# Kernel optimization log

Measured on AMD Instinct MI355X. Metric: run time of the kernel, lower is better.

Reference implementation:

```python
import jax, jax.numpy as jnp
import numpy as np

N_NODES = 8192
N_EDGES = 524288
N_PAIRS = 262144
N_TYPES = 86


def _gcn_conv(x, W, b, src, dst, n):
    # PyG GCNConv: transform, add self-loops, symmetric degree normalization,
    # scatter-add aggregation at destination nodes.
    xw = x @ W  # [N, F_out]
    loop = jnp.arange(n, dtype=src.dtype)
    s = jnp.concatenate([src, loop])
    d = jnp.concatenate([dst, loop])
    deg = jax.ops.segment_sum(jnp.ones(d.shape, xw.dtype), d, num_segments=n)
    dinv = jnp.where(deg > 0, jax.lax.rsqrt(deg), 0.0)  # deg^{-1/2}, 0 for isolated
    coef = dinv[s] * dinv[d]  # [E+N]
    out = jax.ops.segment_sum(xw[s] * coef[:, None], d, num_segments=n)
    return out + b


def setup_inputs() -> dict:
    key = jax.random.key(0)
    ks = jax.random.split(key, 10)
    x = jax.random.normal(ks[0], (N_NODES, N_NODES), dtype=jnp.float32)
    edge_index = jax.random.randint(ks[1], (2, N_EDGES), 0, N_NODES, dtype=jnp.int32)
    drug1_idx = jax.random.randint(ks[2], (N_PAIRS,), 0, N_NODES, dtype=jnp.int32)
    drug2_idx = jax.random.randint(ks[3], (N_PAIRS,), 0, N_NODES, dtype=jnp.int32)
    W1 = jax.random.normal(ks[4], (N_NODES, 128), dtype=jnp.float32) / np.sqrt(N_NODES)
    b1 = jnp.zeros((128,), jnp.float32)
    W2 = jax.random.normal(ks[5], (128, 64), dtype=jnp.float32) / np.sqrt(128.0)
    b2 = jnp.zeros((64,), jnp.float32)
    Wfc = jax.random.normal(ks[6], (128, N_TYPES), dtype=jnp.float32) / np.sqrt(128.0)
    bfc = jnp.zeros((N_TYPES,), jnp.float32)
    return {"x": x, "edge_index": edge_index, "drug1_idx": drug1_idx,
            "drug2_idx": drug2_idx, "W1": W1, "b1": b1, "W2": W2, "b2": b2,
            "Wfc": Wfc, "bfc": bfc}


def reference(x, edge_index, drug1_idx, drug2_idx, W1, b1, W2, b2, Wfc, bfc):
    n = x.shape[0]
    src, dst = edge_index[0], edge_index[1]
    h = jax.nn.relu(_gcn_conv(x, W1, b1, src, dst, n))
    # dropout p=0.3 is identity at inference (training=False)
    h = jax.nn.relu(_gcn_conv(h, W2, b2, src, dst, n))
    combined = jnp.concatenate([h[drug1_idx], h[drug2_idx]], axis=1)  # [P, 128]
    return jax.nn.sigmoid(combined @ Wfc + bfc)
```

## Files before the change

### kernel.cpp

```cpp
#include <hip/hip_runtime.h>
#include <math.h>
#include <stdint.h>
#include <stddef.h>

#define N_NODES 8192
#define N_EDGES 524288
#define N_PAIRS 262144
#define N_TYPES 86
#define F1 128
#define F2 64

typedef unsigned short ushort_t;
typedef unsigned int uint_t;
typedef __attribute__((ext_vector_type(8))) short bfrag;
typedef __attribute__((ext_vector_type(4))) float ffrag;

typedef __attribute__((address_space(3))) char lds_char;
typedef __attribute__((address_space(1))) const char g_char;

__device__ __forceinline__ void gload16(const void* g, void* l) {
  __builtin_amdgcn_global_load_lds((const g_char*)g, (lds_char*)l, 16, 0, 0);
}

__device__ inline ushort_t f2bf(float f) {
  uint_t u = __float_as_uint(f);
  uint_t r = u + 0x7fffu + ((u >> 16) & 1u);
  return (ushort_t)(r >> 16);
}
__device__ inline float bf2f(ushort_t h) {
  return __uint_as_float(((uint_t)h) << 16);
}


__global__ void zero_k(int* __restrict__ p) {
  p[blockIdx.x * 256 + threadIdx.x] = 0;
}

__global__ void count_deg_k(const int* __restrict__ dst, int* __restrict__ cnt) {
  int e = blockIdx.x * blockDim.x + threadIdx.x;
  if (e < N_EDGES) atomicAdd(&cnt[dst[e]], 1);
}

__global__ void scan_k(const int* __restrict__ cnt, int* __restrict__ rp,
                       int* __restrict__ fill, float* __restrict__ dinv) {
  __shared__ int s[1024];
  int t = threadIdx.x;
  int v[8];
  int sum = 0;
#pragma unroll
  for (int i = 0; i < 8; i++) {
    v[i] = cnt[t * 8 + i];
    dinv[t * 8 + i] = 1.0f / sqrtf((float)(v[i] + 1));
    sum += v[i];
  }
  s[t] = sum;
  __syncthreads();
  for (int off = 1; off < 1024; off <<= 1) {
    int add = (t >= off) ? s[t - off] : 0;
    __syncthreads();
    s[t] += add;
    __syncthreads();
  }
  int excl = s[t] - sum;
#pragma unroll
  for (int i = 0; i < 8; i++) {
    rp[t * 8 + i] = excl;
    fill[t * 8 + i] = excl;
    excl += v[i];
  }
  if (t == 1023) rp[N_NODES] = excl;
}

__global__ void scatter_k(const int* __restrict__ src, const int* __restrict__ dst,
                          int* fill, int* __restrict__ csr) {
  int e = blockIdx.x * blockDim.x + threadIdx.x;
  if (e < N_EDGES) {
    int d = dst[e];
    int pos = atomicAdd(&fill[d], 1);
    csr[pos] = src[e];
  }
}


__global__ __launch_bounds__(256) void w1split_k(const float* __restrict__ W1,
                                                 ushort_t* __restrict__ W1th,
                                                 ushort_t* __restrict__ W1tl) {
  __shared__ ushort_t lh[32 * 65];
  __shared__ ushort_t ll[32 * 65];
  int tid = threadIdx.x;
  int k0 = blockIdx.x * 64;
  int n0 = blockIdx.y * 32;
#pragma unroll
  for (int i = 0; i < 8; i++) {
    int c = tid + 256 * i;
    int kr = c >> 5, nc = c & 31;
    float v = W1[(size_t)(k0 + kr) * F1 + n0 + nc];
    ushort_t h = f2bf(v);
    ushort_t l = f2bf(v - bf2f(h));
    lh[nc * 65 + kr] = h;
    ll[nc * 65 + kr] = l;
  }
  __syncthreads();
#pragma unroll
  for (int i = 0; i < 2; i++) {
    int c = tid + 256 * i;
    int buf = c >> 8;
    int cc = c & 255;
    int nr = cc >> 3, kc = cc & 7;
    const ushort_t* l = buf ? ll : lh;
    uint4 u;
    u.x = (uint_t)l[nr * 65 + kc * 8 + 0] | ((uint_t)l[nr * 65 + kc * 8 + 1] << 16);
    u.y = (uint_t)l[nr * 65 + kc * 8 + 2] | ((uint_t)l[nr * 65 + kc * 8 + 3] << 16);
    u.z = (uint_t)l[nr * 65 + kc * 8 + 4] | ((uint_t)l[nr * 65 + kc * 8 + 5] << 16);
    u.w = (uint_t)l[nr * 65 + kc * 8 + 6] | ((uint_t)l[nr * 65 + kc * 8 + 7] << 16);
    ushort_t* dst = (buf ? W1tl : W1th) + (size_t)(n0 + nr) * N_NODES + k0 + kc * 8;
    *(uint4*)dst = u;
  }
}


#define OAH 0
#define OAL 4096
#define OBB(b) (8192 + (b) * 16384)

#define SCHED0 __builtin_amdgcn_sched_barrier(0)
#define WAITVM(N)  do { asm volatile("s_waitcnt vmcnt(" #N ")" ::: "memory"); SCHED0; } while (0)
#define WAITVML(N) do { asm volatile("s_waitcnt vmcnt(" #N ") lgkmcnt(0)" ::: "memory"); SCHED0; } while (0)

__global__ __launch_bounds__(256, 4) void gemm1_mfma_k(const float* __restrict__ x,
                                                       const ushort_t* __restrict__ W1th,
                                                       const ushort_t* __restrict__ W1tl,
                                                       float* __restrict__ part, int kspan) {
  __shared__ __align__(16) char lds[40960];
  int tid = threadIdx.x;
  int wave = tid >> 6, lane = tid & 63;
  int wr = wave >> 1, wc = wave & 1;
  int lrow = lane & 15, kgrp = lane >> 4;
  int m_blk = blockIdx.y * 64;
  int kbase = blockIdx.x * kspan;
  int ktiles = kspan >> 5;

  int bq = wave;
  int b_row = bq * 32 + (lane >> 2);
  int b_kel = ((lane & 3) ^ ((lane >> 2) & 3)) << 3;

  ffrag acc[2][4];
#pragma unroll
  for (int mi = 0; mi < 2; mi++)
#pragma unroll
    for (int ni = 0; ni < 4; ni++) acc[mi][ni] = (ffrag)(0.0f);

  float4 av[2];

#define LOADA(K0)                                                                    \
  {                                                                                  \
    _Pragma("unroll") for (int i = 0; i < 2; i++) {                                  \
      int c = tid + 256 * i;                                                         \
      int row = c >> 3, c4 = c & 7;                                                  \
      av[i] = *(const float4*)&x[(size_t)(m_blk + row) * N_NODES + (K0) + 4 * c4];   \
    }                                                                                \
  }

#define ISSUE_B(K0, BSEL)                                                            \
  {                                                                                  \
    _Pragma("unroll") for (int i = 0; i < 2; i++) {                                  \
      const ushort_t* gh = W1th + (size_t)(b_row + i * 16) * N_NODES + (K0) + b_kel; \
      gload16(gh, lds + OBB(BSEL) + bq * 2048 + i * 1024);                           \
      const ushort_t* gl = W1tl + (size_t)(b_row + i * 16) * N_NODES + (K0) + b_kel; \
      gload16(gl, lds + OBB(BSEL) + 8192 + bq * 2048 + i * 1024);                    \
    }                                                                                \
  }

#define STOREA()                                                                     \
  {                                                                                  \
    _Pragma("unroll") for (int i = 0; i < 2; i++) {                                  \
      int c = tid + 256 * i;                                                         \
      int row = c >> 3, c4 = c & 7;                                                  \
      float f0 = av[i].x, f1 = av[i].y, f2 = av[i].z, f3 = av[i].w;                  \
      ushort_t h0 = f2bf(f0), h1 = f2bf(f1), h2 = f2bf(f2), h3 = f2bf(f3);           \
      ushort_t l0 = f2bf(f0 - bf2f(h0)), l1 = f2bf(f1 - bf2f(h1));                   \
      ushort_t l2 = f2bf(f2 - bf2f(h2)), l3 = f2bf(f3 - bf2f(h3));                   \
      uint2 hp, lp;                                                                  \
      hp.x = (uint_t)h0 | ((uint_t)h1 << 16); hp.y = (uint_t)h2 | ((uint_t)h3 << 16);\
      lp.x = (uint_t)l0 | ((uint_t)l1 << 16); lp.y = (uint_t)l2 | ((uint_t)l3 << 16);\
      uint_t off = row * 64 + ((c4 * 8) ^ ((row & 3) << 4));                         \
      *(uint2*)(lds + OAH + off) = hp;                                               \
      *(uint2*)(lds + OAL + off) = lp;                                               \
    }                                                                                \
  }

#define COMPUTE(BSEL)                                                                \
  {                                                                                  \
    bfrag bh[4], bl[4];                                                              \
    _Pragma("unroll") for (int ni = 0; ni < 4; ni++) {                               \
      int brow = wc * 64 + ni * 16 + lrow;                                           \
      uint_t boff = brow * 64 + ((kgrp * 16) ^ ((brow & 3) << 4));                   \
      bh[ni] = *(const bfrag*)(lds + OBB(BSEL) + boff);                              \
      bl[ni] = *(const bfrag*)(lds + OBB(BSEL) + 8192 + boff);                       \
    }                                                                                \
    _Pragma("unroll") for (int mi = 0; mi < 2; mi++) {                               \
      int arow = wr * 32 + mi * 16 + lrow;                                           \
      uint_t aoff = arow * 64 + ((kgrp * 16) ^ ((arow & 3) << 4));                   \
      bfrag ah = *(const bfrag*)(lds + OAH + aoff);                                  \
      bfrag al = *(const bfrag*)(lds + OAL + aoff);                                  \
      _Pragma("unroll") for (int ni = 0; ni < 4; ni++) {                             \
        acc[mi][ni] = __builtin_amdgcn_mfma_f32_16x16x32_bf16(ah, bh[ni], acc[mi][ni], 0, 0, 0); \
        acc[mi][ni] = __builtin_amdgcn_mfma_f32_16x16x32_bf16(ah, bl[ni], acc[mi][ni], 0, 0, 0); \
        acc[mi][ni] = __builtin_amdgcn_mfma_f32_16x16x32_bf16(al, bh[ni], acc[mi][ni], 0, 0, 0); \
      }                                                                              \
    }                                                                                \
  }

  LOADA(kbase);
  ISSUE_B(kbase, 0);
  WAITVM(4);
  STOREA();
  WAITVML(0);
  __builtin_amdgcn_s_barrier();
  SCHED0;

  for (int s = 0; s < ktiles; ++s) {
    int more = (s + 1 < ktiles);
    if (more) {
      int k0n = kbase + ((s + 1) << 5);
      LOADA(k0n);
      SCHED0;
      ISSUE_B(k0n, (s + 1) & 1);
      SCHED0;
    }
    __builtin_amdgcn_s_setprio(1);
    COMPUTE(s & 1);
    __builtin_amdgcn_s_setprio(0);
    __builtin_amdgcn_s_barrier();
    SCHED0;
    if (more) {
      WAITVM(4);
      STOREA();
      WAITVML(0);
      __builtin_amdgcn_s_barrier();
      SCHED0;
    }
  }

  float* outp = part + (size_t)blockIdx.x * (N_NODES * F1);
#pragma unroll
  for (int mi = 0; mi < 2; mi++) {
#pragma unroll
    for (int ni = 0; ni < 4; ni++) {
      int col = wc * 64 + ni * 16 + lrow;
#pragma unroll
      for (int r = 0; r < 4; r++) {
        int row = m_blk + wr * 32 + mi * 16 + kgrp * 4 + r;
        outp[(size_t)row * F1 + col] = acc[mi][ni][r];
      }
    }
  }
#undef LOADA
#undef ISSUE_B
#undef STOREA
#undef COMPUTE
}

__global__ void reduceS_k(const float* __restrict__ part, float* __restrict__ xw1, int S) {
  int i = blockIdx.x * blockDim.x + threadIdx.x;
  float4 a = ((const float4*)part)[i];
  for (int s = 1; s < S; s++) {
    float4 b = ((const float4*)(part + (size_t)s * N_NODES * F1))[i];
    a.x += b.x; a.y += b.y; a.z += b.z; a.w += b.w;
  }
  ((float4*)xw1)[i] = a;
}


template <int F>
__global__ void agg_k(const float* __restrict__ xw, const int* __restrict__ csr,
                      const int* __restrict__ rp, const float* __restrict__ dinv,
                      const float* __restrict__ bias, float* __restrict__ hout) {
  int node = blockIdx.x;
  int f = threadIdx.x;
  __shared__ int sidx[F];
  __shared__ float sdv[F];
  int beg = rp[node], end = rp[node + 1];
  float acc = 0.f;
  for (int base = beg; base < end; base += F) {
    int n = end - base;
    if (n > F) n = F;
    __syncthreads();
    if (f < n) {
      int s = csr[base + f];
      sidx[f] = s;
      sdv[f] = dinv[s];
    }
    __syncthreads();
    for (int i = 0; i < n; i++) acc += xw[(size_t)sidx[i] * F + f] * sdv[i];
  }
  float dv = dinv[node];
  float v = (acc + xw[(size_t)node * F + f] * dv) * dv + bias[f];
  hout[(size_t)node * F + f] = v > 0.f ? v : 0.f;
}


__global__ __launch_bounds__(256) void gemm2_k(const float* __restrict__ h1,
                                               const float* __restrict__ W2,
                                               float* __restrict__ xw2) {
  __shared__ float W2s[F1 * F2];
  __shared__ float As[16 * F1];
  int tid = threadIdx.x;
  int r0 = blockIdx.x * 16;
#pragma unroll
  for (int j = 0; j < 8; j++)
    ((float4*)W2s)[tid + 256 * j] = ((const float4*)W2)[tid + 256 * j];
#pragma unroll
  for (int j = 0; j < 2; j++)
    ((float4*)As)[tid + 256 * j] = ((const float4*)(h1 + (size_t)r0 * F1))[tid + 256 * j];
  __syncthreads();
  int r = tid >> 4, c4 = tid & 15;
  float4 acc = make_float4(0.f, 0.f, 0.f, 0.f);
#pragma unroll 8
  for (int k = 0; k < F1; k++) {
    float a = As[r * F1 + k];
    float4 bv = *(float4*)&W2s[k * F2 + 4 * c4];
    acc.x += a * bv.x; acc.y += a * bv.y; acc.z += a * bv.z; acc.w += a * bv.w;
  }
  *(float4*)&xw2[(size_t)(r0 + r) * F2 + 4 * c4] = acc;
}


__global__ void pboth_k(const float* __restrict__ h2, const float* __restrict__ Wfc,
                        float* __restrict__ P) {
  __shared__ float hs[64 * 16];
  int tid = threadIdx.x;
  int r0 = blockIdx.x * 16;
  for (int idx = tid; idx < 256; idx += 192) {
    int row = idx >> 4, k4 = idx & 15;
    float4 h = *(const float4*)&h2[(size_t)(r0 + row) * F2 + 4 * k4];
    hs[(4 * k4 + 0) * 16 + row] = h.x;
    hs[(4 * k4 + 1) * 16 + row] = h.y;
    hs[(4 * k4 + 2) * 16 + row] = h.z;
    hs[(4 * k4 + 3) * 16 + row] = h.w;
  }
  __syncthreads();
  if (tid < 172) {
    int half = tid < 86 ? 0 : 1;
    int j = tid - 86 * half;
    const float* wp = Wfc + (size_t)(64 * half) * N_TYPES + j;
    float acc[16];
#pragma unroll
    for (int r = 0; r < 16; r++) acc[r] = 0.f;
    for (int k = 0; k < 64; k++) {
      float w = wp[(size_t)k * N_TYPES];
      const float* hk = &hs[k * 16];
#pragma unroll
      for (int r = 0; r < 16; r++) acc[r] += hk[r] * w;
    }
#pragma unroll
    for (int r = 0; r < 16; r++) P[(size_t)(r0 + r) * 172 + tid] = acc[r];
  }
}


__global__ void final_k(const float* __restrict__ P, const int* __restrict__ d1,
                        const int* __restrict__ d2, const float* __restrict__ bfc,
                        float* __restrict__ out) {
  int gid = blockIdx.x * blockDim.x + threadIdx.x;
  if (gid >= N_PAIRS * 43) return;
  int p = gid / 43;
  int j = gid - p * 43;
  int a = d1[p], b = d2[p];
  float2 v1 = *(const float2*)&P[(size_t)a * 172 + 2 * j];
  float2 v2 = *(const float2*)&P[(size_t)b * 172 + 86 + 2 * j];
  float2 bb = *(const float2*)&bfc[2 * j];
  float z0 = v1.x + v2.x + bb.x;
  float z1 = v1.y + v2.y + bb.y;
  float2 o;
  o.x = 1.0f / (1.0f + expf(-z0));
  o.y = 1.0f / (1.0f + expf(-z1));
  *(float2*)&out[(size_t)p * 86 + 2 * j] = o;
}


extern "C" void kernel_launch(void* const* d_in, const int* in_sizes, int n_in,
                              void* d_out, int out_size, void* d_ws, size_t ws_size,
                              hipStream_t stream) {
  const float* x   = (const float*)d_in[0];
  const int*   ei  = (const int*)d_in[1];
  const int*   d1  = (const int*)d_in[2];
  const int*   d2  = (const int*)d_in[3];
  const float* W1  = (const float*)d_in[4];
  const float* b1  = (const float*)d_in[5];
  const float* W2  = (const float*)d_in[6];
  const float* b2  = (const float*)d_in[7];
  const float* Wfc = (const float*)d_in[8];
  const float* bfc = (const float*)d_in[9];
  float* out = (float*)d_out;

  const int* esrc = ei;
  const int* edst = ei + N_EDGES;

  char* w = (char*)d_ws;
  size_t off = 0;
  auto alloc = [&](size_t bytes) -> char* {
    char* p = w + off;
    off += (bytes + 255) & ~(size_t)255;
    return p;
  };
  int*      cnt  = (int*)alloc((size_t)N_NODES * 4);
  float*    dinv = (float*)alloc((size_t)N_NODES * 4);
  int*      rp   = (int*)alloc((size_t)(N_NODES + 1) * 4);
  int*      fill = (int*)alloc((size_t)N_NODES * 4);
  int*      csr  = (int*)alloc((size_t)N_EDGES * 4);
  ushort_t* W1th = (ushort_t*)alloc((size_t)N_NODES * F1 * 2);
  ushort_t* W1tl = (ushort_t*)alloc((size_t)N_NODES * F1 * 2);
  float*    h1   = (float*)alloc((size_t)N_NODES * F1 * 4);
  float*    xw2  = (float*)alloc((size_t)N_NODES * F2 * 4);
  float*    h2   = (float*)alloc((size_t)N_NODES * F2 * 4);
  float*    P    = (float*)alloc((size_t)N_NODES * 172 * 4);

  size_t partBytes = (size_t)N_NODES * F1 * 4;
  int S = 8;
  while (S > 1 && off + (size_t)S * partBytes > ws_size) S >>= 1;
  float* part = (float*)alloc((size_t)S * partBytes);
  float* xw1 = part;
  if (off > ws_size) return;

  zero_k<<<N_NODES / 256, 256, 0, stream>>>(cnt);
  count_deg_k<<<N_EDGES / 256, 256, 0, stream>>>(edst, cnt);
  scan_k<<<1, 1024, 0, stream>>>(cnt, rp, fill, dinv);
  scatter_k<<<N_EDGES / 256, 256, 0, stream>>>(esrc, edst, fill, csr);

  w1split_k<<<dim3(N_NODES / 64, F1 / 32), 256, 0, stream>>>(W1, W1th, W1tl);
  gemm1_mfma_k<<<dim3(S, N_NODES / 64), 256, 0, stream>>>(x, W1th, W1tl, part, N_NODES / S);
  if (S > 1)
    reduceS_k<<<(N_NODES * F1 / 4) / 256, 256, 0, stream>>>(part, xw1, S);
  agg_k<F1><<<N_NODES, F1, 0, stream>>>(xw1, csr, rp, dinv, b1, h1);

  gemm2_k<<<N_NODES / 16, 256, 0, stream>>>(h1, W2, xw2);
  agg_k<F2><<<N_NODES, F2, 0, stream>>>(xw2, csr, rp, dinv, b2, h2);

  pboth_k<<<N_NODES / 16, 192, 0, stream>>>(h2, Wfc, P);
  final_k<<<(N_PAIRS * 43 + 255) / 256, 256, 0, stream>>>(P, d1, d2, bfc, out);
}
```

Before: 286.0 us.

## Restructure gemm1 into 128-wide K groups with 4-deep B pipeline

The first GEMM now uses 32-row M tiles and loads A in 128-wide K groups, splitting each to bf16 hi/lo once per group. B tiles go into four LDS slots that are prefetched asynchronously, which cuts barriers and lets global loads overlap several compute steps. Each block's starting K group is rotated by block index to spread memory traffic. The cost is twice the LDS (lower occupancy, launch bounds 2) and a grid twice as large, so the W1 B tiles are reloaded by more blocks.

```diff
diff --git a/kernel.cpp b/kernel.cpp
--- a/kernel.cpp
+++ b/kernel.cpp
@@ -119,91 +119,99 @@
 }
 
 
-#define OAH 0
-#define OAL 4096
-#define OBB(b) (8192 + (b) * 16384)
+#define ALDS_H 0
+#define ALDS_L 8192
+#define BLDS(j) (16384 + ((j) & 3) * 16384)
 
 #define SCHED0 __builtin_amdgcn_sched_barrier(0)
 #define WAITVM(N)  do { asm volatile("s_waitcnt vmcnt(" #N ")" ::: "memory"); SCHED0; } while (0)
-#define WAITVML(N) do { asm volatile("s_waitcnt vmcnt(" #N ") lgkmcnt(0)" ::: "memory"); SCHED0; } while (0)
-
-__global__ __launch_bounds__(256, 4) void gemm1_mfma_k(const float* __restrict__ x,
+#define WAITLG     do { asm volatile("s_waitcnt lgkmcnt(0)" ::: "memory"); SCHED0; } while (0)
+
+__global__ __launch_bounds__(256, 2) void gemm1_mfma_k(const float* __restrict__ x,
                                                        const ushort_t* __restrict__ W1th,
                                                        const ushort_t* __restrict__ W1tl,
                                                        float* __restrict__ part, int kspan) {
-  __shared__ __align__(16) char lds[40960];
+  __shared__ __align__(16) char lds[81920];
   int tid = threadIdx.x;
   int wave = tid >> 6, lane = tid & 63;
-  int wr = wave >> 1, wc = wave & 1;
   int lrow = lane & 15, kgrp = lane >> 4;
-  int m_blk = blockIdx.y * 64;
+  int m_blk = blockIdx.y * 32;
   int kbase = blockIdx.x * kspan;
-  int ktiles = kspan >> 5;
+  int ngroups = kspan >> 7;
+  int gmask = ngroups - 1;
+  int g0 = (5 * blockIdx.y + 3 * blockIdx.x) & gmask;
+
+  int ar = tid >> 3, ac = tid & 7;
+  const float* abase = x + (size_t)(m_blk + ar) * N_NODES + ac * 16;
 
   int bq = wave;
   int b_row = bq * 32 + (lane >> 2);
   int b_kel = ((lane & 3) ^ ((lane >> 2) & 3)) << 3;
 
-  ffrag acc[2][4];
+  ffrag acc[2][2];
 #pragma unroll
   for (int mi = 0; mi < 2; mi++)
 #pragma unroll
-    for (int ni = 0; ni < 4; ni++) acc[mi][ni] = (ffrag)(0.0f);
-
-  float4 av[2];
-
-#define LOADA(K0)                                                                    \
+    for (int ni = 0; ni < 2; ni++) acc[mi][ni] = (ffrag)(0.0f);
+
+  float4 av[4];
+
+#define ISSUE_A(WG)                                                                  \
   {                                                                                  \
-    _Pragma("unroll") for (int i = 0; i < 2; i++) {                                  \
-      int c = tid + 256 * i;                                                         \
-      int row = c >> 3, c4 = c & 7;                                                  \
-      av[i] = *(const float4*)&x[(size_t)(m_blk + row) * N_NODES + (K0) + 4 * c4];   \
-    }                                                                                \
-  }
-
-#define ISSUE_B(K0, BSEL)                                                            \
+    const float* p_ = abase + (size_t)(kbase + (WG) * 128);                          \
+    av[0] = *(const float4*)(p_ + 0);                                                \
+    av[1] = *(const float4*)(p_ + 4);                                                \
+    av[2] = *(const float4*)(p_ + 8);                                                \
+    av[3] = *(const float4*)(p_ + 12);                                               \
+  }
+
+#define ISSUE_B(K0, J)                                                               \
   {                                                                                  \
     _Pragma("unroll") for (int i = 0; i < 2; i++) {                                  \
       const ushort_t* gh = W1th + (size_t)(b_row + i * 16) * N_NODES + (K0) + b_kel; \
-      gload16(gh, lds + OBB(BSEL) + bq * 2048 + i * 1024);                           \
+      gload16(gh, lds + BLDS(J) + bq * 2048 + i * 1024);                             \
       const ushort_t* gl = W1tl + (size_t)(b_row + i * 16) * N_NODES + (K0) + b_kel; \
-      gload16(gl, lds + OBB(BSEL) + 8192 + bq * 2048 + i * 1024);                    \
+      gload16(gl, lds + BLDS(J) + 8192 + bq * 2048 + i * 1024);                      \
     }                                                                                \
   }
+
+#define PACKH(a, b) make_uint4(                                                      \
+    (uint_t)f2bf(a.x) | ((uint_t)f2bf(a.y) << 16),                                   \
+    (uint_t)f2bf(a.z) | ((uint_t)f2bf(a.w) << 16),                                   \
+    (uint_t)f2bf(b.x) | ((uint_t)f2bf(b.y) << 16),                                   \
+    (uint_t)f2bf(b.z) | ((uint_t)f2bf(b.w) << 16))
+
+#define PACKL(a, b) make_uint4(                                                      \
+    (uint_t)f2bf(a.x - bf2f(f2bf(a.x))) | ((uint_t)f2bf(a.y - bf2f(f2bf(a.y))) << 16), \
+    (uint_t)f2bf(a.z - bf2f(f2bf(a.z))) | ((uint_t)f2bf(a.w - bf2f(f2bf(a.w))) << 16), \
+    (uint_t)f2bf(b.x - bf2f(f2bf(b.x))) | ((uint_t)f2bf(b.y - bf2f(f2bf(b.y))) << 16), \
+    (uint_t)f2bf(b.z - bf2f(f2bf(b.z))) | ((uint_t)f2bf(b.w - bf2f(f2bf(b.w))) << 16))
 
 #define STOREA()                                                                     \
   {                                                                                  \
-    _Pragma("unroll") for (int i = 0; i < 2; i++) {                                  \
-      int c = tid + 256 * i;                                                         \
-      int row = c >> 3, c4 = c & 7;                                                  \
-      float f0 = av[i].x, f1 = av[i].y, f2 = av[i].z, f3 = av[i].w;                  \
-      ushort_t h0 = f2bf(f0), h1 = f2bf(f1), h2 = f2bf(f2), h3 = f2bf(f3);           \
-      ushort_t l0 = f2bf(f0 - bf2f(h0)), l1 = f2bf(f1 - bf2f(h1));                   \
-      ushort_t l2 = f2bf(f2 - bf2f(h2)), l3 = f2bf(f3 - bf2f(h3));                   \
-      uint2 hp, lp;                                                                  \
-      hp.x = (uint_t)h0 | ((uint_t)h1 << 16); hp.y = (uint_t)h2 | ((uint_t)h3 << 16);\
-      lp.x = (uint_t)l0 | ((uint_t)l1 << 16); lp.y = (uint_t)l2 | ((uint_t)l3 << 16);\
-      uint_t off = row * 64 + ((c4 * 8) ^ ((row & 3) << 4));                         \
-      *(uint2*)(lds + OAH + off) = hp;                                               \
-      *(uint2*)(lds + OAL + off) = lp;                                               \
-    }                                                                                \
-  }
-
-#define COMPUTE(BSEL)                                                                \
+    uint_t o0 = ar * 256 + ((((ac * 2) ^ (ar & 15))) << 4);                          \
+    uint_t o1 = ar * 256 + ((((ac * 2 + 1) ^ (ar & 15))) << 4);                      \
+    *(uint4*)(lds + ALDS_H + o0) = PACKH(av[0], av[1]);                              \
+    *(uint4*)(lds + ALDS_H + o1) = PACKH(av[2], av[3]);                              \
+    *(uint4*)(lds + ALDS_L + o0) = PACKL(av[0], av[1]);                              \
+    *(uint4*)(lds + ALDS_L + o1) = PACKL(av[2], av[3]);                              \
+  }
+
+#define COMPUTE(J)                                                                   \
   {                                                                                  \
-    bfrag bh[4], bl[4];                                                              \
-    _Pragma("unroll") for (int ni = 0; ni < 4; ni++) {                               \
-      int brow = wc * 64 + ni * 16 + lrow;                                           \
+    bfrag bh[2], bl[2];                                                              \
+    _Pragma("unroll") for (int ni = 0; ni < 2; ni++) {                               \
+      int brow = wave * 32 + ni * 16 + lrow;                                         \
       uint_t boff = brow * 64 + ((kgrp * 16) ^ ((brow & 3) << 4));                   \
-      bh[ni] = *(const bfrag*)(lds + OBB(BSEL) + boff);                              \
-      bl[ni] = *(const bfrag*)(lds + OBB(BSEL) + 8192 + boff);                       \
+      bh[ni] = *(const bfrag*)(lds + BLDS(J) + boff);                                \
+      bl[ni] = *(const bfrag*)(lds + BLDS(J) + 8192 + boff);                         \
     }                                                                                \
     _Pragma("unroll") for (int mi = 0; mi < 2; mi++) {                               \
-      int arow = wr * 32 + mi * 16 + lrow;                                           \
-      uint_t aoff = arow * 64 + ((kgrp * 16) ^ ((arow & 3) << 4));                   \
-      bfrag ah = *(const bfrag*)(lds + OAH + aoff);                                  \
-      bfrag al = *(const bfrag*)(lds + OAL + aoff);                                  \
-      _Pragma("unroll") for (int ni = 0; ni < 4; ni++) {                             \
+      int arw = mi * 16 + lrow;                                                      \
+      uint_t aoff = arw * 256 + (((((J) * 4 + kgrp) ^ (arw & 15))) << 4);            \
+      bfrag ah = *(const bfrag*)(lds + ALDS_H + aoff);                               \
+      bfrag al = *(const bfrag*)(lds + ALDS_L + aoff);                               \
+      _Pragma("unroll") for (int ni = 0; ni < 2; ni++) {                             \
         acc[mi][ni] = __builtin_amdgcn_mfma_f32_16x16x32_bf16(ah, bh[ni], acc[mi][ni], 0, 0, 0); \
         acc[mi][ni] = __builtin_amdgcn_mfma_f32_16x16x32_bf16(ah, bl[ni], acc[mi][ni], 0, 0, 0); \
         acc[mi][ni] = __builtin_amdgcn_mfma_f32_16x16x32_bf16(al, bh[ni], acc[mi][ni], 0, 0, 0); \
@@ -211,32 +219,65 @@
     }                                                                                \
   }
 
-  LOADA(kbase);
-  ISSUE_B(kbase, 0);
-  WAITVM(4);
-  STOREA();
-  WAITVML(0);
-  __builtin_amdgcn_s_barrier();
-  SCHED0;
-
-  for (int s = 0; s < ktiles; ++s) {
-    int more = (s + 1 < ktiles);
-    if (more) {
-      int k0n = kbase + ((s + 1) << 5);
-      LOADA(k0n);
-      SCHED0;
-      ISSUE_B(k0n, (s + 1) & 1);
-      SCHED0;
-    }
+#define KB(WG, J) (kbase + (WG) * 128 + (J) * 32)
+
+  {
+    int wg = g0;
+    ISSUE_B(KB(wg, 0), 0);
+    SCHED0;
+    ISSUE_A(wg);
+    SCHED0;
+    WAITVM(0);
+    STOREA();
+    int wgn = (g0 + 1) & gmask;
+    ISSUE_B(KB(wg, 1), 1);
+    ISSUE_B(KB(wg, 2), 2);
+    ISSUE_B(KB(wg, 3), 3);
+    SCHED0;
+    ISSUE_A(wgn);
+    SCHED0;
+    WAITLG;
+    __builtin_amdgcn_s_barrier();
+    SCHED0;
+  }
+
+  for (int g = 0; g < ngroups; ++g) {
+    int wgn = (g0 + g + 1) & gmask;
     __builtin_amdgcn_s_setprio(1);
-    COMPUTE(s & 1);
+    COMPUTE(0);
+    __builtin_amdgcn_s_setprio(0);
+    WAITVM(12);
+    __builtin_amdgcn_s_barrier();
+    SCHED0;
+    ISSUE_B(KB(wgn, 0), 0);
+    SCHED0;
+    __builtin_amdgcn_s_setprio(1);
+    COMPUTE(1);
+    __builtin_amdgcn_s_setprio(0);
+    WAITVM(12);
+    __builtin_amdgcn_s_barrier();
+    SCHED0;
+    __builtin_amdgcn_s_setprio(1);
+    COMPUTE(2);
+    __builtin_amdgcn_s_setprio(0);
+    WAITVM(8);
+    __builtin_amdgcn_s_barrier();
+    SCHED0;
+    __builtin_amdgcn_s_setprio(1);
+    COMPUTE(3);
     __builtin_amdgcn_s_setprio(0);
     __builtin_amdgcn_s_barrier();
     SCHED0;
-    if (more) {
-      WAITVM(4);
+    if (g + 1 < ngroups) {
+      WAITVM(0);
       STOREA();
-      WAITVML(0);
+      ISSUE_B(KB(wgn, 1), 1);
+      ISSUE_B(KB(wgn, 2), 2);
+      ISSUE_B(KB(wgn, 3), 3);
+      SCHED0;
+      ISSUE_A((g0 + g + 2) & gmask);
+      SCHED0;
+      WAITLG;
       __builtin_amdgcn_s_barrier();
       SCHED0;
     }
@@ -246,19 +287,22 @@
 #pragma unroll
   for (int mi = 0; mi < 2; mi++) {
 #pragma unroll
-    for (int ni = 0; ni < 4; ni++) {
-      int col = wc * 64 + ni * 16 + lrow;
+    for (int ni = 0; ni < 2; ni++) {
+      int col = wave * 32 + ni * 16 + lrow;
 #pragma unroll
       for (int r = 0; r < 4; r++) {
-        int row = m_blk + wr * 32 + mi * 16 + kgrp * 4 + r;
+        int row = m_blk + mi * 16 + kgrp * 4 + r;
         outp[(size_t)row * F1 + col] = acc[mi][ni][r];
       }
     }
   }
-#undef LOADA
+#undef ISSUE_A
 #undef ISSUE_B
 #undef STOREA
 #undef COMPUTE
+#undef KB
+#undef PACKH
+#undef PACKL
 }
 
 __global__ void reduceS_k(const float* __restrict__ part, float* __restrict__ xw1, int S) {
@@ -429,7 +473,7 @@
   scatter_k<<<N_EDGES / 256, 256, 0, stream>>>(esrc, edst, fill, csr);
 
   w1split_k<<<dim3(N_NODES / 64, F1 / 32), 256, 0, stream>>>(W1, W1th, W1tl);
-  gemm1_mfma_k<<<dim3(S, N_NODES / 64), 256, 0, stream>>>(x, W1th, W1tl, part, N_NODES / S);
+  gemm1_mfma_k<<<dim3(S, N_NODES / 32), 256, 0, stream>>>(x, W1th, W1tl, part, N_NODES / S);
   if (S > 1)
     reduceS_k<<<(N_NODES * F1 / 4) / 256, 256, 0, stream>>>(part, xw1, S);
   agg_k<F1><<<N_NODES, F1, 0, stream>>>(xw1, csr, rp, dinv, b1, h1);
```

Result: no change. 286.0 us (+0.0%).
